# Optimization experiments

Hardware: AMD Instinct MI355X
Metric: run time of the kernel (lower is better)

The kernel has to match this reference:

```python
import jax, jax.numpy as jnp
import numpy as np

B, NPG, DIN, ED, DEG = 16, 1024, 16, 8, 32
HEADS, OUT1 = 5, 6
HID = HEADS * OUT1          # 30 features after conv1
C1, C2 = 32, 4              # DIFFPool cluster counts
N = B * NPG                 # 16384 total nodes
E = N * DEG                 # 524288 edges


def _egat_conv(x, src, dst, eattr, W, a_s, a_d, We, heads, outc, n_nodes):
    # Edge-gated GAT: per-edge attention logits from src/dst node features plus
    # a linear projection of edge attributes, segment-softmax over incoming edges.
    h = (x @ W).reshape(n_nodes, heads, outc)
    logit = jax.nn.leaky_relu((h[src] * a_s).sum(-1) + (h[dst] * a_d).sum(-1) + eattr @ We, 0.2)  # [E, heads]
    m = jax.ops.segment_max(logit, dst, num_segments=n_nodes)
    ex = jnp.exp(logit - m[dst])
    den = jax.ops.segment_sum(ex, dst, num_segments=n_nodes)
    alpha = ex / (den[dst] + 1e-16)
    out = jax.ops.segment_sum(alpha[:, :, None] * h[src], dst, num_segments=n_nodes)
    return out.reshape(n_nodes, heads * outc), alpha


def _diff_pool(x, adj, s_logits, b, n, c, d):
    s = jax.nn.softmax(s_logits.reshape(b, n, c), axis=-1)
    xp = jnp.einsum('bnc,bnd->bcd', s, x.reshape(b, n, d))
    adjp = jnp.einsum('bnc,bnm,bmk->bck', s, adj, s)
    reg = jnp.mean((adj - jnp.einsum('bnc,bmc->bnm', s, s)) ** 2)  # link-pred loss
    return xp.reshape(b * c, d), adjp, reg


def _dense_edges(b, c):
    base = jnp.arange(c)
    off = (jnp.arange(b) * c)[:, None]
    src = (jnp.repeat(base, c)[None, :] + off).reshape(-1)
    dst = (jnp.tile(base, c)[None, :] + off).reshape(-1)
    return src, dst


def _forward(x, edge_index, edge_attr, adj, params):
    (W1, a_src1, a_dst1, We1, Wp1, as_p1, ad_p1, Wep1,
     Wp2, as_p2, ad_p2, Wep2, Wf1, bf1, Wf2, bf2) = params
    src, dst = edge_index[0], edge_index[1]
    x1, e = _egat_conv(x, src, dst, edge_attr, W1, a_src1, a_dst1, We1, HEADS, OUT1, N)  # [N,30]
    e_dot = jnp.prod(e, axis=-1)[:, None]  # _EGATConv.dot: product over heads (unused downstream)
    s1, _ = _egat_conv(x1, src, dst, edge_attr, Wp1, as_p1, ad_p1, Wep1, 1, C1, N)
    x2, adj2, reg1 = _diff_pool(x1, adj, s1, B, NPG, C1, HID)
    src2, dst2 = _dense_edges(B, C1)
    ea2 = adj2.reshape(B * C1 * C1, 1)  # pooled graph is dense; adj values as edge attrs
    s2, _ = _egat_conv(x2, src2, dst2, ea2, Wp2, as_p2, ad_p2, Wep2, 1, C2, B * C1)
    x3, _, reg2 = _diff_pool(x2, adj2, s2, B, C1, C2, HID)
    reg = reg1 * 10.0 + reg2 * 0.1
    z = x3.reshape(B, C2 * HID)
    z = jax.nn.relu(z @ Wf1 + bf1)
    logits = z @ Wf2 + bf2
    return logits, reg


def setup_inputs() -> dict:
    key = jax.random.key(0)
    ks = jax.random.split(key, 20)
    # block-diagonal random edges: each graph has NPG*DEG edges within its block
    src_l = jax.random.randint(ks[0], (B, NPG * DEG), 0, NPG)
    dst_l = jax.random.randint(ks[1], (B, NPG * DEG), 0, NPG)
    off = (jnp.arange(B) * NPG)[:, None]
    edge_index = jnp.stack([(src_l + off).reshape(-1), (dst_l + off).reshape(-1)])
    adj = jnp.zeros((B, NPG, NPG), jnp.float32).at[jnp.arange(B)[:, None], src_l, dst_l].set(1.0)
    edge_attr = jax.random.uniform(ks[2], (E, ED), jnp.float32)
    x = jax.random.normal(ks[3], (N, DIN), jnp.float32)
    y = jax.random.randint(ks[4], (B,), 0, 2)

    def nrm(k, shape, fan):
        return jax.random.normal(k, shape, jnp.float32) / np.float32(np.sqrt(fan))

    return dict(
        x=x, edge_index=edge_index, edge_attr=edge_attr, y=y, adj=adj,
        W1=nrm(ks[5], (DIN, HEADS * OUT1), DIN),
        a_src1=nrm(ks[6], (HEADS, OUT1), OUT1),
        a_dst1=nrm(ks[7], (HEADS, OUT1), OUT1),
        We1=nrm(ks[8], (ED, HEADS), ED),
        Wp1=nrm(ks[9], (HID, C1), HID),
        as_p1=nrm(ks[10], (1, C1), C1),
        ad_p1=nrm(ks[11], (1, C1), C1),
        Wep1=nrm(ks[12], (ED, 1), ED),
        Wp2=nrm(ks[13], (HID, C2), HID),
        as_p2=nrm(ks[14], (1, C2), C2),
        ad_p2=nrm(ks[15], (1, C2), C2),
        Wep2=nrm(ks[16], (1, 1), 1),
        Wf1=nrm(ks[17], (C2 * HID, 32), C2 * HID),
        bf1=jnp.zeros((32,), jnp.float32),
        Wf2=nrm(ks[18], (32, 2), 32),
        bf2=jnp.zeros((2,), jnp.float32),
    )


def reference(x, edge_index, edge_attr, y, adj, W1, a_src1, a_dst1, We1, Wp1, as_p1, ad_p1, Wep1, Wp2, as_p2, ad_p2, Wep2, Wf1, bf1, Wf2, bf2):
    params = (W1, a_src1, a_dst1, We1, Wp1, as_p1, ad_p1, Wep1,
              Wp2, as_p2, ad_p2, Wep2, Wf1, bf1, Wf2, bf2)
    return _forward(x, edge_index, edge_attr, adj, params)
```

## Files before the change

kernel.cpp:

```cpp
#include <hip/hip_runtime.h>
#include <math.h>

#define NB 16
#define NPG 1024
#define DIN 16
#define ED 8
#define NHEADS 5
#define OUT1 6
#define HID 30
#define C1 32
#define C2 4
#define NN (NB*NPG)
#define EE (NN*32)
#define EPG 32768
#define CH 16
#define CE 2048

__device__ __forceinline__ float lrelu(float v){ return v >= 0.f ? v : 0.2f*v; }

__device__ __forceinline__ void chunk_gc(int& g, int& c){
    int x = blockIdx.x & 7;
    int j = blockIdx.x >> 3;
    g = x + 8*(j >> 4);
    c = j & 15;
}

__device__ __forceinline__ size_t xcd_chunk_base(){
    int x = blockIdx.x & 7;
    int j = blockIdx.x >> 3;
    int g = x + 8*(j >> 7);
    int c = j & 127;
    return (size_t)g*EPG + (size_t)c*256;
}

__global__ void k_hist_chunk(const int* __restrict__ src, const int* __restrict__ dst,
                             int* __restrict__ histD, int* __restrict__ histS,
                             const float* __restrict__ x, const float* __restrict__ W1,
                             const float* __restrict__ as1, const float* __restrict__ ad1,
                             float* __restrict__ h1, float* __restrict__ hs1, float* __restrict__ hd1){
    int t = threadIdx.x;
    if (blockIdx.x < 256){
        __shared__ int hD[NPG], hS[NPG];
        for (int i = t; i < NPG; i += 256){ hD[i] = 0; hS[i] = 0; }
        __syncthreads();
        int g, c; chunk_gc(g, c);
        size_t e0 = ((size_t)g*CH + c)*CE;
        #pragma unroll
        for (int i = 0; i < 8; i++){
            size_t e = e0 + i*256 + t;
            atomicAdd(&hD[dst[e] & (NPG-1)], 1);
            atomicAdd(&hS[src[e] & (NPG-1)], 1);
        }
        __syncthreads();
        size_t hb = ((size_t)g*CH + c)*NPG;
        for (int i = t; i < NPG; i += 256){
            histD[hb + i] = hD[i];
            histS[hb + i] = hS[i];
        }
        return;
    }
    __shared__ float Ws[DIN*HID];
    __shared__ float as_s[HID], ad_s[HID];
    for (int i = t; i < DIN*HID; i += blockDim.x) Ws[i] = W1[i];
    if (t < HID){ as_s[t] = as1[t]; ad_s[t] = ad1[t]; }
    __syncthreads();
    int n = (blockIdx.x - 256)*blockDim.x + t;
    if (n >= NN) return;
    float xv[DIN];
    #pragma unroll
    for (int i = 0; i < DIN; i++) xv[i] = x[n*DIN + i];
    float hv[HID];
    #pragma unroll
    for (int j = 0; j < HID; j++){
        float a = 0.f;
        #pragma unroll
        for (int i = 0; i < DIN; i++) a += xv[i]*Ws[i*HID + j];
        hv[j] = a; h1[(size_t)n*HID + j] = a;
    }
    #pragma unroll
    for (int h = 0; h < NHEADS; h++){
        float s = 0.f, d = 0.f;
        #pragma unroll
        for (int c2 = 0; c2 < OUT1; c2++){ s += hv[h*OUT1+c2]*as_s[h*OUT1+c2]; d += hv[h*OUT1+c2]*ad_s[h*OUT1+c2]; }
        hs1[n*NHEADS + h] = s; hd1[n*NHEADS + h] = d;
    }
}

__global__ __launch_bounds__(1024) void k_cumscan(int* __restrict__ histD, int* __restrict__ histS,
                                                  int* __restrict__ rowptr, int* __restrict__ rowptrS){
    __shared__ int wtot[16], wbase[16];
    bool isD = (blockIdx.x < NB);
    int b = isD ? blockIdx.x : (blockIdx.x - NB);
    int* hist = isD ? histD : histS;
    int* rp   = isD ? rowptr : rowptrS;
    int n = threadIdx.x;
    int run = 0;
    #pragma unroll
    for (int c = 0; c < CH; c++){
        size_t idx = ((size_t)b*CH + c)*NPG + n;
        int v = hist[idx];
        hist[idx] = run;
        run += v;
    }
    int lane = n & 63, wv = n >> 6;
    int sincl = run;
    #pragma unroll
    for (int off = 1; off < 64; off <<= 1){
        int v = __shfl_up(sincl, off, 64);
        if (lane >= off) sincl += v;
    }
    if (lane == 63) wtot[wv] = sincl;
    __syncthreads();
    if (n == 0){
        int r = 0;
        #pragma unroll
        for (int w = 0; w < 16; w++){ wbase[w] = r; r += wtot[w]; }
    }
    __syncthreads();
    int excl = wbase[wv] + sincl - run;
    rp[b*NPG + n] = b*EPG + excl;
    if (b == NB-1 && n == NPG-1) rp[NN] = EE;
}

__global__ void k_scatter_det(const int* __restrict__ src, const int* __restrict__ dst,
                              const int* __restrict__ rowptr, const int* __restrict__ rowptrS,
                              const int* __restrict__ histD, const int* __restrict__ histS,
                              int* __restrict__ srcs, int* __restrict__ eid,
                              int* __restrict__ dsts, int* __restrict__ nbrS){
    __shared__ int baseD[NPG], baseS[NPG];
    int t = threadIdx.x;
    int g, c; chunk_gc(g, c);
    size_t hb = ((size_t)g*CH + c)*NPG;
    for (int i = t; i < NPG; i += 256){
        baseD[i] = rowptr[g*NPG + i] + histD[hb + i];
        baseS[i] = rowptrS[g*NPG + i] + histS[hb + i];
    }
    __syncthreads();
    size_t e0 = ((size_t)g*CH + c)*CE;
    #pragma unroll
    for (int i = 0; i < 8; i++){
        size_t e = e0 + i*256 + t;
        int s = src[e], d = dst[e];
        int p = atomicAdd(&baseD[d & (NPG-1)], 1);
        srcs[p] = s; eid[p] = (int)e; dsts[p] = d;
        int pS = atomicAdd(&baseS[s & (NPG-1)], 1);
        nbrS[pS] = d;
    }
}

__global__ void k_elogit(const float* __restrict__ ea, const float* __restrict__ We1,
                         const float* __restrict__ Wep1,
                         const int* __restrict__ srcs, const int* __restrict__ eid,
                         const int* __restrict__ dsts,
                         const float* __restrict__ hs1, const float* __restrict__ hd1,
                         float* __restrict__ lg1T, float* __restrict__ ewp1s){
    __shared__ float W[ED*NHEADS];
    __shared__ float Wp[ED];
    int t = threadIdx.x;
    if (t < ED*NHEADS) W[t] = We1[t];
    if (t < ED) Wp[t] = Wep1[t];
    __syncthreads();
    size_t k = xcd_chunk_base() + t;
    int s = srcs[k], e = eid[k], d = dsts[k];
    float a[ED];
    #pragma unroll
    for (int i = 0; i < ED; i++) a[i] = ea[(size_t)e*ED + i];
    const float* hsr = hs1 + (size_t)s*NHEADS;
    const float* hdr = hd1 + (size_t)d*NHEADS;
    #pragma unroll
    for (int h = 0; h < NHEADS; h++){
        float sv = 0.f;
        #pragma unroll
        for (int i = 0; i < ED; i++) sv += a[i]*W[i*NHEADS + h];
        lg1T[(size_t)h*EE + k] = lrelu(hsr[h] + hdr[h] + sv);
    }
    float sv = 0.f;
    #pragma unroll
    for (int i = 0; i < ED; i++) sv += a[i]*Wp[i];
    ewp1s[k] = sv;
}

__global__ void k_conv1_agg(const int* __restrict__ srcs, const int* __restrict__ rowptr,
                            const float* __restrict__ h1, const float* __restrict__ lg1T,
                            float* __restrict__ x1){
    int tid = blockIdx.x*blockDim.x + threadIdx.x;
    if (tid >= NN*NHEADS*4) return;
    int n = tid / (NHEADS*4);
    int r = tid - n*(NHEADS*4);
    int h = r >> 2;
    int q = (r >> 1) & 1;
    int eh = r & 1;
    int k0 = rowptr[n], k1 = rowptr[n+1];
    int mid = k0 + ((k1 - k0 + 1) >> 1);
    int ka = eh ? mid : k0;
    int kb = eh ? k1 : mid;
    const float* lgh = lg1T + (size_t)h*EE;
    float m = -INFINITY, den = 0.f;
    float acc[3] = {0.f, 0.f, 0.f};
    int k = ka;
    for (; k + 4 <= kb; k += 4){
        float l0 = lgh[k+0], l1 = lgh[k+1], l2 = lgh[k+2], l3 = lgh[k+3];
        int s0 = srcs[k+0], s1 = srcs[k+1], s2 = srcs[k+2], s3 = srcs[k+3];
        const float* p0 = h1 + (size_t)s0*HID + h*OUT1 + q*3;
        const float* p1 = h1 + (size_t)s1*HID + h*OUT1 + q*3;
        const float* p2 = h1 + (size_t)s2*HID + h*OUT1 + q*3;
        const float* p3 = h1 + (size_t)s3*HID + h*OUT1 + q*3;
        float mb = fmaxf(fmaxf(l0, l1), fmaxf(l2, l3));
        float mn = fmaxf(m, mb);
        float f  = expf(m - mn);
        float e0 = expf(l0 - mn), e1 = expf(l1 - mn);
        float e2 = expf(l2 - mn), e3 = expf(l3 - mn);
        m = mn;
        den = den*f + e0 + e1 + e2 + e3;
        #pragma unroll
        for (int c = 0; c < 3; c++)
            acc[c] = acc[c]*f + e0*p0[c] + e1*p1[c] + e2*p2[c] + e3*p3[c];
    }
    for (; k < kb; k++){
        float l = lgh[k];
        int s = srcs[k];
        float mn = fmaxf(m, l);
        float f  = expf(m - mn);
        float ex = expf(l - mn);
        m = mn;
        den = den*f + ex;
        const float* hr = h1 + (size_t)s*HID + h*OUT1 + q*3;
        #pragma unroll
        for (int c = 0; c < 3; c++) acc[c] = acc[c]*f + ex*hr[c];
    }
    float mo  = __shfl_xor(m, 1, 64);
    float dno = __shfl_xor(den, 1, 64);
    float ao0 = __shfl_xor(acc[0], 1, 64);
    float ao1 = __shfl_xor(acc[1], 1, 64);
    float ao2 = __shfl_xor(acc[2], 1, 64);
    float M = fmaxf(m, mo);
    float f1 = (m  == -INFINITY) ? 0.f : expf(m  - M);
    float f2 = (mo == -INFINITY) ? 0.f : expf(mo - M);
    float DEN = den*f1 + dno*f2;
    if (eh == 0){
        float inv = 1.f / (DEN + 1e-16f);
        x1[(size_t)n*HID + h*OUT1 + q*3 + 0] = (acc[0]*f1 + ao0*f2)*inv;
        x1[(size_t)n*HID + h*OUT1 + q*3 + 1] = (acc[1]*f1 + ao1*f2)*inv;
        x1[(size_t)n*HID + h*OUT1 + q*3 + 2] = (acc[2]*f1 + ao2*f2)*inv;
    }
}

__global__ void k_pd(const float* __restrict__ x1, const float* __restrict__ Wp1,
                     const float* __restrict__ asp, const float* __restrict__ adp,
                     float* __restrict__ hp1, float* __restrict__ hsp, float* __restrict__ hdp,
                     const int* __restrict__ rowptrS, const int* __restrict__ nbrS,
                     int* __restrict__ unbr, int* __restrict__ ucnt,
                     float* __restrict__ scal){
    __shared__ float Ws[HID*C1];
    __shared__ float as_s[C1], ad_s[C1];
    __shared__ unsigned int bm[256*33];
    __shared__ int red[256];
    int t = threadIdx.x;
    if (blockIdx.x < 64){
        for (int i = t; i < HID*C1; i += blockDim.x) Ws[i] = Wp1[i];
        if (t < C1){ as_s[t] = asp[t]; ad_s[t] = adp[t]; }
        __syncthreads();
        int n = blockIdx.x*blockDim.x + t;
        float xv[HID];
        #pragma unroll
        for (int d = 0; d < HID; d++) xv[d] = x1[(size_t)n*HID + d];
        float s = 0.f, dd = 0.f;
        for (int c = 0; c < C1; c++){
            float a = 0.f;
            #pragma unroll
            for (int d = 0; d < HID; d++) a += xv[d]*Ws[d*C1 + c];
            hp1[(size_t)n*C1 + c] = a;
            s += a*as_s[c]; dd += a*ad_s[c];
        }
        hsp[n] = s; hdp[n] = dd;
        return;
    }
    unsigned int* mybm = &bm[t*33];
    #pragma unroll
    for (int i = 0; i < 32; i++) mybm[i] = 0u;
    int n = (blockIdx.x - 64)*blockDim.x + t;
    int cnt = 0;
    {
        int k0 = rowptrS[n], k1 = rowptrS[n+1];
        for (int k = k0; k < k1; k++){
            int m = nbrS[k];
            int loc = m & (NPG-1);
            unsigned int w = (unsigned int)(loc >> 5);
            unsigned int bit = 1u << (loc & 31);
            unsigned int old = mybm[w];
            if (!(old & bit)){
                mybm[w] = old | bit;
                unbr[k0 + cnt] = m;
                cnt++;
            }
        }
        ucnt[n] = cnt;
    }
    red[t] = cnt; __syncthreads();
    for (int s = 128; s > 0; s >>= 1){ if (t < s) red[t] += red[t+s]; __syncthreads(); }
    if (t == 0) atomicAdd(&scal[0], (float)red[0]);
}

__global__ void k_plogit(const int* __restrict__ srcs, const int* __restrict__ dsts,
                         const float* __restrict__ hsp, const float* __restrict__ hdp,
                         const float* __restrict__ ewp1s, float* __restrict__ lgp){
    size_t k = xcd_chunk_base() + threadIdx.x;
    lgp[k] = lrelu(hsp[srcs[k]] + hdp[dsts[k]] + ewp1s[k]);
}

__global__ void k_pool1_agg(const int* __restrict__ srcs, const int* __restrict__ rowptr,
                            const float* __restrict__ hp1, const float* __restrict__ lgp,
                            float* __restrict__ ssoft){
    __shared__ float sm[16*33];
    int tid = blockIdx.x*blockDim.x + threadIdx.x;
    int r = tid & 15;
    int q = r >> 1;
    int eh = r & 1;
    int n = tid >> 4;
    int nl = threadIdx.x >> 4;
    int k0 = rowptr[n], k1 = rowptr[n+1];
    int mid = k0 + ((k1 - k0 + 1) >> 1);
    int ka = eh ? mid : k0;
    int kb = eh ? k1 : mid;
    float m = -INFINITY, den = 0.f;
    float acc[4] = {0.f, 0.f, 0.f, 0.f};
    int k = ka;
    for (; k + 4 <= kb; k += 4){
        float l0 = lgp[k+0], l1 = lgp[k+1], l2 = lgp[k+2], l3 = lgp[k+3];
        int s0 = srcs[k+0], s1n = srcs[k+1], s2 = srcs[k+2], s3 = srcs[k+3];
        float4 v0 = *(const float4*)(hp1 + (size_t)s0*C1 + q*4);
        float4 v1 = *(const float4*)(hp1 + (size_t)s1n*C1 + q*4);
        float4 v2 = *(const float4*)(hp1 + (size_t)s2*C1 + q*4);
        float4 v3 = *(const float4*)(hp1 + (size_t)s3*C1 + q*4);
        float mb = fmaxf(fmaxf(l0, l1), fmaxf(l2, l3));
        float mn = fmaxf(m, mb);
        float f  = expf(m - mn);
        float e0 = expf(l0 - mn), e1 = expf(l1 - mn);
        float e2 = expf(l2 - mn), e3 = expf(l3 - mn);
        m = mn;
        den = den*f + e0 + e1 + e2 + e3;
        acc[0] = acc[0]*f + e0*v0.x + e1*v1.x + e2*v2.x + e3*v3.x;
        acc[1] = acc[1]*f + e0*v0.y + e1*v1.y + e2*v2.y + e3*v3.y;
        acc[2] = acc[2]*f + e0*v0.z + e1*v1.z + e2*v2.z + e3*v3.z;
        acc[3] = acc[3]*f + e0*v0.w + e1*v1.w + e2*v2.w + e3*v3.w;
    }
    for (; k < kb; k++){
        float l = lgp[k];
        int s = srcs[k];
        float mn = fmaxf(m, l);
        float f  = expf(m - mn);
        float ex = expf(l - mn);
        m = mn;
        den = den*f + ex;
        const float* hr = hp1 + (size_t)s*C1 + q*4;
        #pragma unroll
        for (int c = 0; c < 4; c++) acc[c] = acc[c]*f + ex*hr[c];
    }
    float mo  = __shfl_xor(m, 1, 64);
    float dno = __shfl_xor(den, 1, 64);
    float ao[4];
    #pragma unroll
    for (int c = 0; c < 4; c++) ao[c] = __shfl_xor(acc[c], 1, 64);
    float M = fmaxf(m, mo);
    float f1 = (m  == -INFINITY) ? 0.f : expf(m  - M);
    float f2 = (mo == -INFINITY) ? 0.f : expf(mo - M);
    float DEN = den*f1 + dno*f2;
    if (eh == 0){
        float inv = 1.f / (DEN + 1e-16f);
        #pragma unroll
        for (int c = 0; c < 4; c++) sm[nl*33 + q*4 + c] = (acc[c]*f1 + ao[c]*f2)*inv;
    }
    __syncthreads();
    float mx = -INFINITY;
    #pragma unroll 8
    for (int i = 0; i < C1; i++) mx = fmaxf(mx, sm[nl*33 + i]);
    float sum = 0.f;
    #pragma unroll 8
    for (int i = 0; i < C1; i++) sum += expf(sm[nl*33 + i] - mx);
    float is = 1.f/sum;
    if (eh == 0){
        #pragma unroll
        for (int c = 0; c < 4; c++)
            ssoft[(size_t)n*C1 + q*4 + c] = expf(sm[nl*33 + q*4 + c] - mx)*is;
    }
}

__global__ void k_T(const int* __restrict__ rowptrS, const int* __restrict__ unbr,
                    const int* __restrict__ ucnt, const float* __restrict__ ssoft,
                    float* __restrict__ T){
    int tid = blockIdx.x*blockDim.x + threadIdx.x;
    int r = tid & 15;
    int q = r >> 1;
    int eh = r & 1;
    int n = tid >> 4;
    int k0 = rowptrS[n];
    int cnt = ucnt[n];
    int half = (cnt + 1) >> 1;
    int ia = eh ? half : 0;
    int ib = eh ? cnt : half;
    float acc[4] = {0.f, 0.f, 0.f, 0.f};
    int i = ia;
    for (; i + 4 <= ib; i += 4){
        int m0 = unbr[k0+i+0], m1 = unbr[k0+i+1], m2 = unbr[k0+i+2], m3 = unbr[k0+i+3];
        float4 v0 = *(const float4*)(ssoft + (size_t)m0*C1 + q*4);
        float4 v1 = *(const float4*)(ssoft + (size_t)m1*C1 + q*4);
        float4 v2 = *(const float4*)(ssoft + (size_t)m2*C1 + q*4);
        float4 v3 = *(const float4*)(ssoft + (size_t)m3*C1 + q*4);
        acc[0] += v0.x + v1.x + v2.x + v3.x;
        acc[1] += v0.y + v1.y + v2.y + v3.y;
        acc[2] += v0.z + v1.z + v2.z + v3.z;
        acc[3] += v0.w + v1.w + v2.w + v3.w;
    }
    for (; i < ib; i++){
        int m = unbr[k0 + i];
        const float* sr = ssoft + (size_t)m*C1 + q*4;
        #pragma unroll
        for (int c = 0; c < 4; c++) acc[c] += sr[c];
    }
    #pragma unroll
    for (int c = 0; c < 4; c++) acc[c] += __shfl_xor(acc[c], 1, 64);
    if (eh == 0){
        #pragma unroll
        for (int c = 0; c < 4; c++) T[(size_t)n*C1 + q*4 + c] = acc[c];
    }
}

__global__ void k_partials(const float* __restrict__ ssoft, const float* __restrict__ T,
                           const float* __restrict__ x1,
                           float* __restrict__ adj2, float* __restrict__ Gm,
                           float* __restrict__ x2){
    int b  = blockIdx.y;
    int n0 = blockIdx.x * 64;
    int t  = threadIdx.x;
    __shared__ float ssh[64*C1];
    __shared__ float tsh[64*C1];
    __shared__ float xsh[64*HID];
    {
        size_t sbase = ((size_t)b*NPG + n0)*C1;
        #pragma unroll
        for (int i = 0; i < 8; i++){
            int lin = t + i*256;
            ssh[lin] = ssoft[sbase + lin];
            tsh[lin] = T[sbase + lin];
        }
        size_t xbase = ((size_t)b*NPG + n0)*HID;
        for (int lin = t; lin < 64*HID; lin += 256) xsh[lin] = x1[xbase + lin];
    }
    __syncthreads();
    float accA[4] = {0,0,0,0}, accG[4] = {0,0,0,0}, accX[4] = {0,0,0,0};
    int cA[4], kA[4], cX[4], dX[4];
    #pragma unroll
    for (int q = 0; q < 4; q++){
        int p = t + q*256;
        cA[q] = p >> 5; kA[q] = p & 31;
        cX[q] = p / HID; dX[q] = p - cX[q]*HID;
    }
    for (int r = 0; r < 64; r++){
        const float* sr = ssh + r*C1;
        const float* tr = tsh + r*C1;
        const float* xr = xsh + r*HID;
        #pragma unroll
        for (int q = 0; q < 4; q++){
            float sc = sr[cA[q]];
            accA[q] += sc*tr[kA[q]];
            accG[q] += sc*sr[kA[q]];
        }
        #pragma unroll
        for (int q = 0; q < 4; q++){
            int p = t + q*256;
            if (p < C1*HID) accX[q] += sr[cX[q]]*xr[dX[q]];
        }
    }
    #pragma unroll
    for (int q = 0; q < 4; q++){
        int p = t + q*256;
        atomicAdd(&adj2[(size_t)b*1024 + p], accA[q]);
        atomicAdd(&Gm[(size_t)b*1024 + p], accG[q]);
        if (p < C1*HID) atomicAdd(&x2[((size_t)b*C1 + cX[q])*HID + dX[q]], accX[q]);
    }
}

__global__ void k_tail(const float* __restrict__ x2, const float* __restrict__ adj2,
                       const float* __restrict__ Gm,
                       const float* __restrict__ Wp2, const float* __restrict__ asp,
                       const float* __restrict__ adp, const float* __restrict__ Wep2,
                       const float* __restrict__ Wf1, const float* __restrict__ bf1,
                       const float* __restrict__ Wf2, const float* __restrict__ bf2,
                       float* __restrict__ out, float* __restrict__ scal,
                       unsigned int* __restrict__ ctr){
    int b = blockIdx.x;
    int t = threadIdx.x;
    __shared__ float x2s[C1*HID];
    __shared__ float a2s[C1*C1];
    __shared__ float Wps[HID*C2];
    __shared__ float h2s[C1*C2];
    __shared__ float hs2s[C1], hd2s[C1];
    __shared__ float sss[C1*C2];
    __shared__ float x3s[C2*HID];
    __shared__ float zsh[32];
    __shared__ float red[256];
    for (int i = t; i < C1*HID; i += 256) x2s[i] = x2[(size_t)b*C1*HID + i];
    for (int i = t; i < C1*C1; i += 256) a2s[i] = adj2[(size_t)b*C1*C1 + i];
    if (t < HID*C2) Wps[t] = Wp2[t];
    __syncthreads();
    {
        float ltr = 0.f, lfr = 0.f;
        for (int p = t; p < 1024; p += 256){
            float g = Gm[(size_t)b*1024 + p];
            lfr += g*g;
            if ((p >> 5) == (p & 31)) ltr += a2s[p];
        }
        red[t] = ltr; __syncthreads();
        for (int s = 128; s > 0; s >>= 1){ if (t < s) red[t] += red[t+s]; __syncthreads(); }
        if (t == 0) atomicAdd(&scal[1], red[0]);
        __syncthreads();
        red[t] = lfr; __syncthreads();
        for (int s = 128; s > 0; s >>= 1){ if (t < s) red[t] += red[t+s]; __syncthreads(); }
        if (t == 0) atomicAdd(&scal[2], red[0]);
        __syncthreads();
    }
    if (t < C1){
        float s = 0.f, dd = 0.f;
        #pragma unroll
        for (int c = 0; c < C2; c++){
            float a = 0.f;
            #pragma unroll
            for (int d = 0; d < HID; d++) a += x2s[t*HID + d]*Wps[d*C2 + c];
            h2s[t*C2 + c] = a;
            s += a*asp[c]; dd += a*adp[c];
        }
        hs2s[t] = s; hd2s[t] = dd;
    }
    __syncthreads();
    if (t < C1){
        int j = t;
        float hdv = hd2s[j];
        float wep = Wep2[0];
        float m = -INFINITY;
        for (int i = 0; i < C1; i++)
            m = fmaxf(m, lrelu(hs2s[i] + hdv + a2s[i*C1 + j]*wep));
        float den = 0.f;
        float acc[C2] = {0,0,0,0};
        for (int i = 0; i < C1; i++){
            float ex = expf(lrelu(hs2s[i] + hdv + a2s[i*C1 + j]*wep) - m);
            den += ex;
            #pragma unroll
            for (int c = 0; c < C2; c++) acc[c] += ex * h2s[i*C2 + c];
        }
        float inv = 1.f/(den + 1e-16f);
        float v[C2]; float mx = -INFINITY;
        #pragma unroll
        for (int c = 0; c < C2; c++){ v[c] = acc[c]*inv; mx = fmaxf(mx, v[c]); }
        float sum = 0.f;
        #pragma unroll
        for (int c = 0; c < C2; c++){ v[c] = expf(v[c] - mx); sum += v[c]; }
        float i2 = 1.f/sum;
        #pragma unroll
        for (int c = 0; c < C2; c++) sss[j*C2 + c] = v[c]*i2;
    }
    __syncthreads();
    if (t < C2*HID){
        int c = t / HID, d = t % HID;
        float a = 0.f;
        #pragma unroll
        for (int n = 0; n < C1; n++) a += sss[n*C2 + c]*x2s[n*HID + d];
        x3s[t] = a;
    }
    {
        float loc = 0.f;
        for (int p = t; p < 1024; p += 256){
            int n = p >> 5, mm = p & 31;
            float dot = 0.f;
            #pragma unroll
            for (int c = 0; c < C2; c++) dot += sss[n*C2 + c]*sss[mm*C2 + c];
            float df = a2s[p] - dot;
            loc += df*df;
        }
        red[t] = loc; __syncthreads();
        for (int s = 128; s > 0; s >>= 1){ if (t < s) red[t] += red[t+s]; __syncthreads(); }
        if (t == 0) atomicAdd(&scal[3], red[0]);
        __syncthreads();
    }
    if (t < 32){
        float a = bf1[t];
        #pragma unroll 4
        for (int k = 0; k < C2*HID; k++) a += x3s[k]*Wf1[k*32 + t];
        zsh[t] = fmaxf(a, 0.f);
    }
    __syncthreads();
    if (t < 2){
        float a = bf2[t];
        #pragma unroll
        for (int j = 0; j < 32; j++) a += zsh[j]*Wf2[j*2 + t];
        out[b*2 + t] = a;
    }
    if (t == 0){
        __threadfence();
        unsigned int old = atomicAdd(ctr, 1u);
        if (old == NB - 1){
            float adjsum = atomicAdd(&scal[0], 0.f);
            float tr     = atomicAdd(&scal[1], 0.f);
            float fr     = atomicAdd(&scal[2], 0.f);
            float r2     = atomicAdd(&scal[3], 0.f);
            float reg1 = (adjsum - 2.f*tr + fr) * (1.f/16777216.f);
            float reg2 = r2 * (1.f/16384.f);
            out[32] = 10.f*reg1 + 0.1f*reg2;
        }
    }
}

extern "C" void kernel_launch(void* const* d_in, const int* in_sizes, int n_in,
                              void* d_out, int out_size, void* d_ws, size_t ws_size,
                              hipStream_t stream) {
    const float* x    = (const float*)d_in[0];
    const int*   ei   = (const int*)d_in[1];
    const float* ea   = (const float*)d_in[2];
    const float* W1   = (const float*)d_in[5];
    const float* as1  = (const float*)d_in[6];
    const float* ad1  = (const float*)d_in[7];
    const float* We1  = (const float*)d_in[8];
    const float* Wp1  = (const float*)d_in[9];
    const float* asp1 = (const float*)d_in[10];
    const float* adp1 = (const float*)d_in[11];
    const float* Wep1 = (const float*)d_in[12];
    const float* Wp2  = (const float*)d_in[13];
    const float* asp2 = (const float*)d_in[14];
    const float* adp2 = (const float*)d_in[15];
    const float* Wep2 = (const float*)d_in[16];
    const float* Wf1  = (const float*)d_in[17];
    const float* bf1  = (const float*)d_in[18];
    const float* Wf2  = (const float*)d_in[19];
    const float* bf2  = (const float*)d_in[20];
    float* out = (float*)d_out;

    const int* srcA = ei;
    const int* dstA = ei + EE;

    char* wp = (char*)d_ws;
    auto carve = [&](size_t bytes)->char*{
        char* p = wp;
        wp += (bytes + 255) & ~(size_t)255;
        return p;
    };
    float* h1    = (float*)carve((size_t)NN*HID*4);
    float* hs1   = (float*)carve((size_t)NN*NHEADS*4);
    float* hd1   = (float*)carve((size_t)NN*NHEADS*4);
    float* lg1T  = (float*)carve((size_t)EE*NHEADS*4);
    float* ewp1s = (float*)carve((size_t)EE*4);
    float* lgp   = (float*)carve((size_t)EE*4);
    float* x1    = (float*)carve((size_t)NN*HID*4);
    float* hp1   = (float*)carve((size_t)NN*C1*4);
    float* hsp   = (float*)carve((size_t)NN*4);
    float* hdp   = (float*)carve((size_t)NN*4);
    float* ssoft = (float*)carve((size_t)NN*C1*4);
    float* T     = (float*)carve((size_t)NN*C1*4);
    float* x2    = (float*)carve((size_t)NB*C1*HID*4);
    float* adj2  = (float*)carve((size_t)NB*C1*C1*4);
    float* Gm    = (float*)carve((size_t)NB*C1*C1*4);
    float* scal  = (float*)carve(16*4);
    unsigned int* ctr = (unsigned int*)(scal + 8);
    int* histD   = (int*)carve((size_t)NB*CH*NPG*4);
    int* histS   = (int*)carve((size_t)NB*CH*NPG*4);
    int* rowptr  = (int*)carve((size_t)(NN+1)*4);
    int* rowptrS = (int*)carve((size_t)(NN+1)*4);
    int* srcs    = (int*)carve((size_t)EE*4);
    int* eid     = (int*)carve((size_t)EE*4);
    int* dsts    = (int*)carve((size_t)EE*4);
    int* nbrS    = (int*)carve((size_t)EE*4);
    int* unbr    = (int*)carve((size_t)EE*4);
    int* ucnt    = (int*)carve((size_t)NN*4);

    hipMemsetAsync(scal, 0, 16*4, stream);
    hipMemsetAsync(x2, 0, (size_t)(NB*C1*HID + 2*NB*C1*C1)*4, stream);

    const int TB = 256;

    k_hist_chunk<<<dim3(256 + 64), TB, 0, stream>>>(srcA, dstA, histD, histS,
                                                    x, W1, as1, ad1, h1, hs1, hd1);
    k_cumscan<<<dim3(2*NB), 1024, 0, stream>>>(histD, histS, rowptr, rowptrS);
    k_scatter_det<<<dim3(256), TB, 0, stream>>>(srcA, dstA, rowptr, rowptrS,
                                                histD, histS, srcs, eid, dsts, nbrS);

    k_elogit<<<dim3(2048), TB, 0, stream>>>(ea, We1, Wep1, srcs, eid, dsts, hs1, hd1, lg1T, ewp1s);

    k_conv1_agg<<<dim3(NN*NHEADS*4/TB), TB, 0, stream>>>(srcs, rowptr, h1, lg1T, x1);

    k_pd<<<dim3(128), TB, 0, stream>>>(x1, Wp1, asp1, adp1, hp1, hsp, hdp,
                                       rowptrS, nbrS, unbr, ucnt, scal);

    k_plogit<<<dim3(2048), TB, 0, stream>>>(srcs, dsts, hsp, hdp, ewp1s, lgp);
    k_pool1_agg<<<dim3(NN*16/TB), TB, 0, stream>>>(srcs, rowptr, hp1, lgp, ssoft);

    k_T<<<dim3(NN*16/TB), TB, 0, stream>>>(rowptrS, unbr, ucnt, ssoft, T);
    k_partials<<<dim3(16, NB), TB, 0, stream>>>(ssoft, T, x1, adj2, Gm, x2);

    k_tail<<<dim3(NB), TB, 0, stream>>>(x2, adj2, Gm, Wp2, asp2, adp2, Wep2,
                                        Wf1, bf1, Wf2, bf2, out, scal, ctr);
}
```

Baseline: 285.8 us.

## Stage per-graph node features in LDS for conv1 aggregation

Each block now handles 64 destination nodes of one graph. It first loads that whole graph's 1024x30 h1 feature table into shared memory, so the neighbour gathers read LDS instead of scattered global memory. This relies on every edge's source lying in the same graph, which is why source ids are masked with NPG-1. The edge-split across paired threads and the shuffle merge are dropped, so each thread walks all of a node's edges. That leaves fewer threads (256 blocks of 640) and adds a 120KB shared buffer per block, which limits occupancy to about one block per CU and adds a bulk load before any work starts.

```diff
diff --git a/kernel.cpp b/kernel.cpp
--- a/kernel.cpp
+++ b/kernel.cpp
@@ -180,31 +180,38 @@
     ewp1s[k] = sv;
 }
 
-__global__ void k_conv1_agg(const int* __restrict__ srcs, const int* __restrict__ rowptr,
+__global__ __launch_bounds__(640) void k_conv1_agg(const int* __restrict__ srcs,
+                            const int* __restrict__ rowptr,
                             const float* __restrict__ h1, const float* __restrict__ lg1T,
                             float* __restrict__ x1){
-    int tid = blockIdx.x*blockDim.x + threadIdx.x;
-    if (tid >= NN*NHEADS*4) return;
-    int n = tid / (NHEADS*4);
-    int r = tid - n*(NHEADS*4);
-    int h = r >> 2;
-    int q = (r >> 1) & 1;
-    int eh = r & 1;
+    __shared__ float hls[NPG*HID];
+    int t = threadIdx.x;
+    int xx = blockIdx.x & 7;
+    int j = blockIdx.x >> 3;
+    int g = xx + 8*(j >> 4);
+    int seg = j & 15;
+    const float* hg = h1 + (size_t)g*NPG*HID;
+    for (int i = t; i < NPG*HID; i += 640) hls[i] = hg[i];
+    __syncthreads();
+    int nl = seg*64 + t/10;
+    int r = t - (t/10)*10;
+    int h = r >> 1;
+    int q = r & 1;
+    int n = g*NPG + nl;
     int k0 = rowptr[n], k1 = rowptr[n+1];
-    int mid = k0 + ((k1 - k0 + 1) >> 1);
-    int ka = eh ? mid : k0;
-    int kb = eh ? k1 : mid;
     const float* lgh = lg1T + (size_t)h*EE;
+    int off = h*OUT1 + q*3;
     float m = -INFINITY, den = 0.f;
     float acc[3] = {0.f, 0.f, 0.f};
-    int k = ka;
-    for (; k + 4 <= kb; k += 4){
+    int k = k0;
+    for (; k + 4 <= k1; k += 4){
         float l0 = lgh[k+0], l1 = lgh[k+1], l2 = lgh[k+2], l3 = lgh[k+3];
-        int s0 = srcs[k+0], s1 = srcs[k+1], s2 = srcs[k+2], s3 = srcs[k+3];
-        const float* p0 = h1 + (size_t)s0*HID + h*OUT1 + q*3;
-        const float* p1 = h1 + (size_t)s1*HID + h*OUT1 + q*3;
-        const float* p2 = h1 + (size_t)s2*HID + h*OUT1 + q*3;
-        const float* p3 = h1 + (size_t)s3*HID + h*OUT1 + q*3;
+        int s0 = srcs[k+0] & (NPG-1), s1 = srcs[k+1] & (NPG-1);
+        int s2 = srcs[k+2] & (NPG-1), s3 = srcs[k+3] & (NPG-1);
+        const float* p0 = hls + s0*HID + off;
+        const float* p1 = hls + s1*HID + off;
+        const float* p2 = hls + s2*HID + off;
+        const float* p3 = hls + s3*HID + off;
         float mb = fmaxf(fmaxf(l0, l1), fmaxf(l2, l3));
         float mn = fmaxf(m, mb);
         float f  = expf(m - mn);
@@ -216,33 +223,21 @@
         for (int c = 0; c < 3; c++)
             acc[c] = acc[c]*f + e0*p0[c] + e1*p1[c] + e2*p2[c] + e3*p3[c];
     }
-    for (; k < kb; k++){
+    for (; k < k1; k++){
         float l = lgh[k];
-        int s = srcs[k];
+        int s = srcs[k] & (NPG-1);
         float mn = fmaxf(m, l);
         float f  = expf(m - mn);
         float ex = expf(l - mn);
         m = mn;
         den = den*f + ex;
-        const float* hr = h1 + (size_t)s*HID + h*OUT1 + q*3;
+        const float* hr = hls + s*HID + off;
         #pragma unroll
         for (int c = 0; c < 3; c++) acc[c] = acc[c]*f + ex*hr[c];
     }
-    float mo  = __shfl_xor(m, 1, 64);
-    float dno = __shfl_xor(den, 1, 64);
-    float ao0 = __shfl_xor(acc[0], 1, 64);
-    float ao1 = __shfl_xor(acc[1], 1, 64);
-    float ao2 = __shfl_xor(acc[2], 1, 64);
-    float M = fmaxf(m, mo);
-    float f1 = (m  == -INFINITY) ? 0.f : expf(m  - M);
-    float f2 = (mo == -INFINITY) ? 0.f : expf(mo - M);
-    float DEN = den*f1 + dno*f2;
-    if (eh == 0){
-        float inv = 1.f / (DEN + 1e-16f);
-        x1[(size_t)n*HID + h*OUT1 + q*3 + 0] = (acc[0]*f1 + ao0*f2)*inv;
-        x1[(size_t)n*HID + h*OUT1 + q*3 + 1] = (acc[1]*f1 + ao1*f2)*inv;
-        x1[(size_t)n*HID + h*OUT1 + q*3 + 2] = (acc[2]*f1 + ao2*f2)*inv;
-    }
+    float inv = 1.f / (den + 1e-16f);
+    #pragma unroll
+    for (int c = 0; c < 3; c++) x1[(size_t)n*HID + off + c] = acc[c]*inv;
 }
 
 __global__ void k_pd(const float* __restrict__ x1, const float* __restrict__ Wp1,
@@ -683,7 +678,7 @@
 
     k_elogit<<<dim3(2048), TB, 0, stream>>>(ea, We1, Wep1, srcs, eid, dsts, hs1, hd1, lg1T, ewp1s);
 
-    k_conv1_agg<<<dim3(NN*NHEADS*4/TB), TB, 0, stream>>>(srcs, rowptr, h1, lg1T, x1);
+    k_conv1_agg<<<dim3(256), 640, 0, stream>>>(srcs, rowptr, h1, lg1T, x1);
 
     k_pd<<<dim3(128), TB, 0, stream>>>(x1, Wp1, asp1, adp1, hp1, hsp, hdp,
                                        rowptrS, nbrS, unbr, ucnt, scal);
```

Result: faster. 280.2 us (-2.0%).
